# Kernel tuning notes

Measured on AMD Instinct MI355X. Metric: run time of the kernel, lower is better.

## Reference

```python
import jax, jax.numpy as jnp
import numpy as np

D_MODEL = 64
D_INNER = 128
D_STATE = 16
D_CONV = 4
DT_RANK = 4
P_PIX = 5
HH = 120
WW = 120


def _layernorm(x, g, b):
    m = x.mean(-1, keepdims=True)
    v = ((x - m) ** 2).mean(-1, keepdims=True)
    return (x - m) * jax.lax.rsqrt(v + 1e-5) * g + b


def _ssm_scan(delta, Bm, Cm, u, A):
    # delta,u: (b,L,d); Bm,Cm: (b,L,n); A: (d,n)
    def step(h, inp):
        dt, bt, ct, ut = inp  # (b,d),(b,n),(b,n),(b,d)
        h = h * jnp.exp(dt[:, :, None] * A) + (dt * ut)[:, :, None] * bt[:, None, :]
        return h, jnp.einsum('bdn,bn->bd', h, ct)
    h0 = jnp.zeros((u.shape[0], A.shape[0], A.shape[1]), u.dtype)
    xs = (jnp.swapaxes(delta, 0, 1), jnp.swapaxes(Bm, 0, 1),
          jnp.swapaxes(Cm, 0, 1), jnp.swapaxes(u, 0, 1))
    _, ys = jax.lax.scan(step, h0, xs)
    return jnp.swapaxes(ys, 0, 1)  # (b,L,d)


def _mamba(p, x):
    # faithful mamba_ssm Mamba with use_fast_path=False, out_proj=Identity
    in_w, conv_w, conv_b, xproj_w, dt_w, dt_b, A_log, Dv = p
    L = x.shape[1]
    xz = jnp.einsum('bld,ed->ble', x, in_w)  # (b,L,2*d_inner)
    xh, z = xz[..., :D_INNER], xz[..., D_INNER:]
    xp = jnp.pad(xh, ((0, 0), (D_CONV - 1, 0), (0, 0)))  # causal depthwise conv
    conv = conv_b + sum(xp[:, i:i + L, :] * conv_w[:, i] for i in range(D_CONV))
    xh = jax.nn.silu(conv)
    dbl = jnp.einsum('bld,ed->ble', xh, xproj_w)
    dt = dbl[..., :DT_RANK]
    Bm = dbl[..., DT_RANK:DT_RANK + D_STATE]
    Cm = dbl[..., DT_RANK + D_STATE:]
    delta = jax.nn.softplus(jnp.einsum('blr,dr->bld', dt, dt_w) + dt_b)
    A = -jnp.exp(A_log)
    y = _ssm_scan(delta, Bm, Cm, xh, A) + xh * Dv
    return y * jax.nn.silu(z)


def _bidir(p2, xn):
    inp = jnp.stack([xn, xn[:, ::-1]])  # forward + flipped sequence
    ys = jax.vmap(_mamba, in_axes=(0, 0))(p2, inp)
    return ys[0], ys[1]


def _pixel(x, p2, g, b, out_w):
    B, C, Hh, Ww = x.shape
    p = P_PIX
    NH, NW = Hh // p, Ww // p
    L = NH * NW
    xd = x.reshape(B, C, NH, p, NW, p).transpose(0, 3, 5, 1, 2, 4).reshape(B * p * p, C, L)
    xn = _layernorm(jnp.swapaxes(xd, 1, 2), g, b)
    yf, yb = _bidir(p2, xn)
    yo = jnp.einsum('bld,cd->blc', yf + yb[:, ::-1], out_w)
    xo = jnp.swapaxes(yo, 1, 2).reshape(B, p, p, C, NH, NW).transpose(0, 3, 4, 1, 5, 2).reshape(B, C, Hh, Ww)
    return xo + x


def _window(x, p2, g, b, out_w, out_bw):
    # window p==1: AvgPool(1)/Upsample(1) are identities
    B, C, Hh, Ww = x.shape
    L = Hh * Ww
    xn = _layernorm(jnp.swapaxes(x.reshape(B, C, L), 1, 2), g, b)
    yf, yb = _bidir(p2, xn)
    xM = jnp.einsum('bld,cd->bcl', yf, out_w)
    yM = jnp.einsum('bld,cd->bcl', yb, out_bw)
    xo = jnp.einsum('bld,cd->blc', yf + yb[:, ::-1], out_w)
    return jnp.swapaxes(xo, 1, 2).reshape(B, C, Hh, Ww) + x, xM, yM


def _edges(M, step=32):
    hub = np.arange(0, M, step)
    ii, jj = np.meshgrid(hub, hub, indexing='ij')
    mask = ii != jj
    # off-diagonal hub-hub edges + self loops for every node (GCNConv add_remaining_self_loops)
    src = np.concatenate([ii[mask], np.arange(M)])
    dst = np.concatenate([jj[mask], np.arange(M)])
    deg = np.bincount(dst, minlength=M).astype(np.float32)
    norm = (deg[src] ** -0.5) * (deg[dst] ** -0.5)
    return jnp.asarray(src), jnp.asarray(dst), jnp.asarray(norm, jnp.float32)


def _gcn(x, Wm, bv, src, dst, norm, M):
    h = jnp.einsum('bmf,gf->bmg', x, Wm)
    msg = h[:, src, :] * norm[None, :, None]          # (B,E,g)
    agg = jax.ops.segment_sum(jnp.swapaxes(msg, 0, 1), dst, num_segments=M)
    return jnp.swapaxes(agg, 0, 1) + bv


def setup_inputs() -> dict:
    key = jax.random.key(0)
    ks = iter(jax.random.split(key, 48))
    def rn(shape, scale=1.0):
        return jax.random.normal(next(ks), shape, jnp.float32) * scale
    d = {}
    d['x'] = rn((1, D_MODEL, HH, WW))
    for pre in ('pix', 'win'):
        d[pre + '_in_w'] = rn((4, 2, 2 * D_INNER, D_MODEL), D_MODEL ** -0.5)
        d[pre + '_conv_w'] = rn((4, 2, D_INNER, D_CONV), 0.3)
        d[pre + '_conv_b'] = rn((4, 2, D_INNER), 0.02)
        d[pre + '_xproj_w'] = rn((4, 2, DT_RANK + 2 * D_STATE, D_INNER), D_INNER ** -0.5)
        d[pre + '_dt_w'] = rn((4, 2, D_INNER, DT_RANK), DT_RANK ** -0.5)
        d[pre + '_dt_b'] = jax.random.uniform(next(ks), (4, 2, D_INNER), jnp.float32, -5.0, -3.0)
        d[pre + '_A_log'] = jnp.log(jax.random.uniform(next(ks), (4, 2, D_INNER, D_STATE), jnp.float32, 1.0, 16.0))
        d[pre + '_D'] = rn((4, 2, D_INNER), 0.5)
        d[pre + '_ln_g'] = jnp.ones((4, D_MODEL), jnp.float32)
        d[pre + '_ln_b'] = jnp.zeros((4, D_MODEL), jnp.float32)
    d['pix_out_w'] = rn((4, D_MODEL, D_INNER), D_INNER ** -0.5)
    d['win_out_w'] = rn((4, D_MODEL, D_INNER), D_INNER ** -0.5)
    d['win_out_bw'] = rn((4, D_MODEL, D_INNER), D_INNER ** -0.5)
    d['gcn_w1'] = rn((2 * D_MODEL, 4 * D_MODEL), (4 * D_MODEL) ** -0.5)
    d['gcn_b1'] = jnp.zeros((2 * D_MODEL,), jnp.float32)
    d['gcn_w2'] = rn((D_MODEL, 2 * D_MODEL), (2 * D_MODEL) ** -0.5)
    d['gcn_b2'] = jnp.zeros((D_MODEL,), jnp.float32)
    return d


def reference(x, pix_in_w, pix_conv_w, pix_conv_b, pix_xproj_w, pix_dt_w, pix_dt_b, pix_A_log, pix_D,
              win_in_w, win_conv_w, win_conv_b, win_xproj_w, win_dt_w, win_dt_b, win_A_log, win_D,
              pix_ln_g, pix_ln_b, win_ln_g, win_ln_b, pix_out_w, win_out_w, win_out_bw,
              gcn_w1, gcn_b1, gcn_w2, gcn_b2):
    pix_stack = (pix_in_w, pix_conv_w, pix_conv_b, pix_xproj_w, pix_dt_w, pix_dt_b, pix_A_log, pix_D)
    win_stack = (win_in_w, win_conv_w, win_conv_b, win_xproj_w, win_dt_w, win_dt_b, win_A_log, win_D)
    def pick(stack, i):
        return tuple(t[i] for t in stack)
    def branch(x0, base):
        lastx, xM, yM = x0, None, None
        for s in range(2):
            i = base + s
            a = _pixel(lastx, pick(pix_stack, i), pix_ln_g[i], pix_ln_b[i], pix_out_w[i])
            a, xM, yM = _window(a, pick(win_stack, i), win_ln_g[i], win_ln_b[i], win_out_w[i], win_out_bw[i])
            lastx = lastx + a
        return lastx, xM, yM
    old = x
    lastx, xM, yM = branch(x, 0)
    lastx_T, xMT, yMT = branch(jnp.swapaxes(x, 2, 3), 2)
    B, C, Hh, Ww = x.shape
    M = Hh * Ww
    nf = jnp.swapaxes(jnp.concatenate([xM, yM, xMT, yMT], axis=1), 1, 2)  # (B,M,4C)
    src, dst, norm = _edges(M)
    h = jax.nn.relu(_gcn(nf, gcn_w1, gcn_b1, src, dst, norm, M))
    g = _gcn(h, gcn_w2, gcn_b2, src, dst, norm, M)
    gcn_x = jnp.swapaxes(g, 1, 2).reshape(B, C, Hh, Ww)
    return gcn_x + old + lastx + jnp.swapaxes(lastx_T, 2, 3)
```

## Files before the change

kernel.cpp:

```cpp
#include <hip/hip_runtime.h>
#include <hip/hip_bf16.h>

#define MT 14400
#define WNC 300
#define WCL 48
#define PT 16

typedef unsigned short u16;

__device__ __forceinline__ float b2f(u16 u){
  union { unsigned int i; float f; } v; v.i = ((unsigned int)u) << 16; return v.f;
}
__device__ __forceinline__ u16 f2b(float f){
  union { unsigned int i; float f; } v; v.f = f;
  unsigned int x = v.i;
  return (u16)((x + 0x7fffu + ((x >> 16) & 1u)) >> 16);
}
__device__ __forceinline__ unsigned int pk2(float a, float b){
  return (unsigned int)f2b(a) | ((unsigned int)f2b(b) << 16);
}
__device__ __forceinline__ void st8(float* p, uint4 v){
  *(float4*)p = make_float4(b2f((u16)v.x), b2f((u16)(v.x >> 16)), b2f((u16)v.y), b2f((u16)(v.y >> 16)));
  *(float4*)(p + 4) = make_float4(b2f((u16)v.z), b2f((u16)(v.z >> 16)), b2f((u16)v.w), b2f((u16)(v.w >> 16)));
}
__device__ __forceinline__ float siluf(float x){ return x / (1.f + expf(-x)); }
__device__ __forceinline__ float softplusf(float x){ return (x > 20.f) ? x : log1pf(expf(x)); }

__global__ __launch_bounds__(256) void k_detect(const u16* __restrict__ a, int n, int* __restrict__ flag){
  __shared__ int found;
  if (threadIdx.x == 0) found = 0;
  __syncthreads();
  int f = 0;
  for (int i = threadIdx.x; i < n; i += 256){
    float v = b2f(a[i]);
    if (!(fabsf(v) <= 1e9f)) f = 1;
  }
  if (f) atomicOr(&found, 1);
  __syncthreads();
  if (threadIdx.x == 0) *flag = found;
}

struct PTab {
  const void* src[27];
  float* dst[27];
  int n[27];
  int neg[27];
};

__global__ __launch_bounds__(256) void k_cvt(PTab tb, const int* __restrict__ flag){
  int id = blockIdx.y;
  int n = tb.n[id];
  int fp32 = *flag;
  float* d = tb.dst[id];
  int ng = tb.neg[id];
  for (int i = blockIdx.x * 256 + threadIdx.x; i < n; i += gridDim.x * 256){
    float v = fp32 ? ((const float*)tb.src[id])[i] : b2f(((const u16*)tb.src[id])[i]);
    if (ng) v = -expf(v) * 1.4426950408889634f;
    d[i] = v;
  }
}

__global__ __launch_bounds__(256) void k_wtrans(const float* __restrict__ Wpix, const float* __restrict__ Wwin,
                                                float* __restrict__ WTpix, float* __restrict__ WTwin){
  int mat = blockIdx.y;
  const float* src = (mat < 8) ? (Wpix + (size_t)mat * 16384) : (Wwin + (size_t)(mat - 8) * 16384);
  float* dst = (mat < 8) ? (WTpix + (size_t)mat * 16384) : (WTwin + (size_t)(mat - 8) * 16384);
  int idx = blockIdx.x * 256 + threadIdx.x;
  int e = idx >> 6, k = idx & 63;
  dst[k * 256 + e] = src[idx];
}

__global__ __launch_bounds__(256) void k_gcn1w(const float* __restrict__ ow, const float* __restrict__ obw,
                                               const float* __restrict__ G1, float* __restrict__ W1c){
  int str = blockIdx.y;
  int g = str >> 1, d = str & 1;
  int i2 = g * 2 + 1;
  const float* W = (d ? obw : ow) + (size_t)(i2 * 64) * 128;
  int idx = blockIdx.x * 256 + threadIdx.x;
  int kk = idx >> 7, f = idx & 127;
  float acc = 0.f;
  #pragma unroll 8
  for (int c = 0; c < 64; c++)
    acc += W[(size_t)c * 128 + kk] * G1[(size_t)f * 256 + str * 64 + c];
  W1c[((size_t)str * 128 + kk) * 128 + f] = acc;
}

__global__ __launch_bounds__(256) void k_cvt_x(const void* __restrict__ x, float* __restrict__ imgA,
                                               const int* __restrict__ flag){
  int idx = blockIdx.x * 256 + threadIdx.x;
  int l = idx % MT, c = idx / MT;
  float v = (*flag) ? ((const float*)x)[idx] : b2f(((const u16*)x)[idx]);
  imgA[idx] = v;
  imgA[(size_t)64 * MT + (size_t)c * MT + (l % 120) * 120 + l / 120] = v;
}

__global__ __launch_bounds__(256) void k_prep_xn(const float* __restrict__ img, const float* __restrict__ lng,
                                                 const float* __restrict__ lnb, u16* __restrict__ xn,
                                                 int s, int pixelMode){
  int tid = threadIdx.x;
  int q = blockIdx.x * 4 + (tid >> 6);
  int c = tid & 63;
  int g = q / MT, t = q % MT;
  int hw;
  if (pixelMode){
    int b = t / 576, l = t % 576;
    int ph = b / 5, pw = b % 5, nh = l / 24, nw = l % 24;
    hw = (nh * 5 + ph) * 120 + (nw * 5 + pw);
  } else hw = t;
  float v = img[(size_t)g * 64 * MT + (size_t)c * MT + hw];
  float sm = v;
  #pragma unroll
  for (int m = 32; m >= 1; m >>= 1) sm += __shfl_xor(sm, m);
  float mean = sm * (1.f / 64.f);
  float dv = v - mean;
  float s2 = dv * dv;
  #pragma unroll
  for (int m = 32; m >= 1; m >>= 1) s2 += __shfl_xor(s2, m);
  float var = s2 * (1.f / 64.f);
  int i2 = g * 2 + s;
  float o = dv * rsqrtf(var + 1e-5f) * lng[i2 * 64 + c] + lnb[i2 * 64 + c];
  xn[(size_t)g * MT * 64 + (size_t)t * 64 + c] = f2b(o);
}

__global__ __launch_bounds__(256) void k_inproj(const u16* __restrict__ xn, const float* __restrict__ WT,
                                                u16* __restrict__ xh, u16* __restrict__ z,
                                                int s, int pixelMode){
  int gd = blockIdx.y, g = gd >> 1, dir = gd & 1;
  int i2 = (g * 2 + s) * 2 + dir;
  int ttile = blockIdx.x >> 1, ntile = blockIdx.x & 1;
  int t0 = ttile * 64;
  const float* WTm = WT + (size_t)i2 * 16384 + ntile * 128;

  __shared__ __align__(16) float sA[64 * 68];
  __shared__ __align__(16) float sB[64 * 128];
  int tid = threadIdx.x;

  {
    int k0 = (tid & 15) * 4;
    #pragma unroll
    for (int it = 0; it < 4; it++){
      int t = (tid >> 4) + it * 16;
      int tq = t0 + t, src = tq;
      if (dir){
        if (pixelMode){ int b = tq / 576, l = tq % 576; src = b * 576 + 575 - l; }
        else src = MT - 1 - tq;
      }
      uint2 v = *(const uint2*)&xn[(size_t)g * MT * 64 + (size_t)src * 64 + k0];
      sA[t * 68 + k0]     = b2f((u16)v.x);
      sA[t * 68 + k0 + 1] = b2f((u16)(v.x >> 16));
      sA[t * 68 + k0 + 2] = b2f((u16)v.y);
      sA[t * 68 + k0 + 3] = b2f((u16)(v.y >> 16));
    }
  }
  {
    #pragma unroll
    for (int it = 0; it < 8; it++){
      int idx = it * 256 + tid;
      int k = idx >> 5, e4 = (idx & 31) * 4;
      float4 v = *(const float4*)&WTm[(size_t)k * 256 + e4];
      *(float4*)&sB[k * 128 + e4] = v;
    }
  }
  __syncthreads();

  int tr = tid >> 4, tc = tid & 15;
  float acc[4][8];
  #pragma unroll
  for (int i = 0; i < 4; i++)
    #pragma unroll
    for (int j = 0; j < 8; j++) acc[i][j] = 0.f;

  for (int k0 = 0; k0 < 64; k0 += 4){
    float4 a4[4];
    #pragma unroll
    for (int i = 0; i < 4; i++) a4[i] = *(const float4*)&sA[(tr * 4 + i) * 68 + k0];
    #pragma unroll
    for (int kk = 0; kk < 4; kk++){
      float4 b0 = *(const float4*)&sB[(k0 + kk) * 128 + tc * 8];
      float4 b1 = *(const float4*)&sB[(k0 + kk) * 128 + tc * 8 + 4];
      float bv[8] = {b0.x, b0.y, b0.z, b0.w, b1.x, b1.y, b1.z, b1.w};
      #pragma unroll
      for (int i = 0; i < 4; i++){
        const float* ap = (const float*)&a4[i];
        float av = ap[kk];
        #pragma unroll
        for (int j = 0; j < 8; j++) acc[i][j] += av * bv[j];
      }
    }
  }

  u16* dst = ntile ? z : xh;
  #pragma unroll
  for (int i = 0; i < 4; i++){
    int t_out = t0 + tr * 4 + i;
    size_t base = (size_t)gd * MT * 128 + (size_t)t_out * 128 + tc * 8;
    uint4 o;
    o.x = pk2(acc[i][0], acc[i][1]); o.y = pk2(acc[i][2], acc[i][3]);
    o.z = pk2(acc[i][4], acc[i][5]); o.w = pk2(acc[i][6], acc[i][7]);
    *(uint4*)&dst[base] = o;
  }
}

__global__ __launch_bounds__(256) void k_conv(const u16* __restrict__ raw, const float* __restrict__ cw,
                                              const float* __restrict__ cb, u16* __restrict__ xhs,
                                              int s, int pixelMode){
  int gd = blockIdx.y, g = gd >> 1, dir = gd & 1;
  int i2 = (g * 2 + s) * 2 + dir;
  int idx = blockIdx.x * 256 + threadIdx.x;
  int t = idx >> 7, ch = idx & 127;
  int SL = pixelMode ? 576 : MT;
  int pos = t % SL;
  const u16* src = raw + (size_t)gd * MT * 128;
  const float* wrow = cw + (size_t)(i2 * 128 + ch) * 4;
  float acc = cb[i2 * 128 + ch];
  #pragma unroll
  for (int i = 0; i < 4; i++){
    int d = 3 - i;
    if (pos >= d) acc += b2f(src[(size_t)(t - d) * 128 + ch]) * wrow[i];
  }
  xhs[(size_t)gd * MT * 128 + idx] = f2b(siluf(acc));
}

__global__ __launch_bounds__(256) void k_xproj(const u16* __restrict__ xhs, const float* __restrict__ xpb,
                                               const float* __restrict__ dtw, const float* __restrict__ dtb,
                                               u16* __restrict__ delta, u16* __restrict__ Bm,
                                               u16* __restrict__ Cm, int s){
  int gd = blockIdx.y, g = gd >> 1, dir = gd & 1;
  int i2 = (g * 2 + s) * 2 + dir;
  const float* XP = xpb + (size_t)i2 * 36 * 128;
  const float* DW = dtw + (size_t)i2 * 128 * 4;
  const float* DB = dtb + (size_t)i2 * 128;
  int t0 = blockIdx.x * 64;
  size_t gb = (size_t)gd * MT * 128;
  size_t gb16 = (size_t)gd * MT * 16;

  __shared__ __align__(16) float sX[64 * 132];
  __shared__ __align__(16) float sW[48 * 132];
  float* sDbl = sX;
  int tid = threadIdx.x;

  #pragma unroll
  for (int it = 0; it < 8; it++){
    int idx = it * 256 + tid;
    int tok = idx >> 5, k4 = (idx & 31) * 4;
    uint2 v = *(const uint2*)&xhs[gb + (size_t)(t0 + tok) * 128 + k4];
    sX[tok * 132 + k4]     = b2f((u16)v.x);
    sX[tok * 132 + k4 + 1] = b2f((u16)(v.x >> 16));
    sX[tok * 132 + k4 + 2] = b2f((u16)v.y);
    sX[tok * 132 + k4 + 3] = b2f((u16)(v.y >> 16));
  }
  for (int idx = tid; idx < 48 * 32; idx += 256){
    int out = idx >> 5, k4 = (idx & 31) * 4;
    float4 v = (out < 36) ? *(const float4*)&XP[(size_t)out * 128 + k4]
                          : make_float4(0.f, 0.f, 0.f, 0.f);
    *(float4*)&sW[out * 132 + k4] = v;
  }
  __syncthreads();

  int tr = tid >> 4, tc = tid & 15;
  float acc[4][3];
  #pragma unroll
  for (int i = 0; i < 4; i++){ acc[i][0]=0.f; acc[i][1]=0.f; acc[i][2]=0.f; }

  for (int k0 = 0; k0 < 128; k0 += 4){
    float4 a4[4], bw[3];
    #pragma unroll
    for (int i = 0; i < 4; i++) a4[i] = *(const float4*)&sX[(tr * 4 + i) * 132 + k0];
    #pragma unroll
    for (int j = 0; j < 3; j++) bw[j] = *(const float4*)&sW[(tc * 3 + j) * 132 + k0];
    #pragma unroll
    for (int kk = 0; kk < 4; kk++){
      #pragma unroll
      for (int i = 0; i < 4; i++){
        float av = ((const float*)&a4[i])[kk];
        #pragma unroll
        for (int j = 0; j < 3; j++) acc[i][j] += av * ((const float*)&bw[j])[kk];
      }
    }
  }
  __syncthreads();

  #pragma unroll
  for (int i = 0; i < 4; i++){
    #pragma unroll
    for (int j = 0; j < 3; j++){
      int out = tc * 3 + j;
      if (out < 36) sDbl[(tr * 4 + i) * 52 + out] = acc[i][j];
    }
  }
  __syncthreads();

  {
    int d = tid & 127, half = tid >> 7;
    float4 dw = *(const float4*)&DW[(size_t)d * 4];
    float db = DB[d];
    #pragma unroll
    for (int it = 0; it < 32; it++){
      int t = it * 2 + half;
      const float* row = &sDbl[t * 52];
      float v = db + row[0] * dw.x + row[1] * dw.y + row[2] * dw.z + row[3] * dw.w;
      delta[gb + (size_t)(t0 + t) * 128 + d] = f2b(softplusf(v));
    }
  }
  #pragma unroll
  for (int it = 0; it < 8; it++){
    int flat = it * 256 + tid;
    int t = flat >> 5, n = flat & 31;
    float v = sDbl[t * 52 + 4 + n];
    if (n < 16) Bm[gb16 + (size_t)(t0 + t) * 16 + n] = f2b(v);
    else        Cm[gb16 + (size_t)(t0 + t) * 16 + (n - 16)] = f2b(v);
  }
}

__global__ __launch_bounds__(256) void k_scan_p1(const u16* __restrict__ delta, const u16* __restrict__ xhs,
                                                 const u16* __restrict__ Bm, const float* __restrict__ A2b,
                                                 float* __restrict__ Acar, float* __restrict__ Bcar, int s){
  int gd = blockIdx.y, g = gd >> 1, dir = gd & 1;
  int i2 = (g * 2 + s) * 2 + dir;
  int chunk = blockIdx.x;
  int tid = threadIdx.x, ch = tid >> 1, nb = (tid & 1) * 8;
  float A2[8], ap[8], bc[8];
  #pragma unroll
  for (int j = 0; j < 8; j++){
    A2[j] = A2b[((size_t)i2 * 128 + ch) * 16 + nb + j];
    ap[j] = 1.f; bc[j] = 0.f;
  }
  size_t so = (size_t)gd * MT * 128 + (size_t)chunk * WCL * 128;
  size_t bo = (size_t)gd * MT * 16  + (size_t)chunk * WCL * 16;
  __shared__ __align__(16) float sd[PT * 128];
  __shared__ __align__(16) float su[PT * 128];
  __shared__ __align__(16) float sb[PT * 16];
  uint4 rd, ru; float rbf;
  rd = *(const uint4*)&delta[so + 8 * (size_t)tid];
  ru = *(const uint4*)&xhs[so + 8 * (size_t)tid];
  rbf = b2f(Bm[bo + tid]);
  const int NT = WCL / PT;
  for (int tile = 0; tile < NT; tile++){
    __syncthreads();
    st8(&sd[8 * tid], rd);
    st8(&su[8 * tid], ru);
    sb[tid] = rbf;
    __syncthreads();
    if (tile + 1 < NT){
      rd = *(const uint4*)&delta[so + (size_t)(tile + 1) * PT * 128 + 8 * (size_t)tid];
      ru = *(const uint4*)&xhs[so + (size_t)(tile + 1) * PT * 128 + 8 * (size_t)tid];
      rbf = b2f(Bm[bo + (size_t)(tile + 1) * PT * 16 + tid]);
    }
    #pragma unroll
    for (int t = 0; t < PT; t++){
      float dt = sd[t * 128 + ch];
      float u  = su[t * 128 + ch];
      float du = dt * u;
      #pragma unroll
      for (int j = 0; j < 8; j++){
        float e = exp2f(dt * A2[j]);
        bc[j] = bc[j] * e + du * sb[t * 16 + nb + j];
        ap[j] *= e;
      }
    }
  }
  size_t o = ((size_t)gd * WNC + chunk) * 2048 + (size_t)ch * 16 + nb;
  float4* A4 = (float4*)(Acar + o);
  float4* B4 = (float4*)(Bcar + o);
  A4[0] = make_float4(ap[0], ap[1], ap[2], ap[3]);
  A4[1] = make_float4(ap[4], ap[5], ap[6], ap[7]);
  B4[0] = make_float4(bc[0], bc[1], bc[2], bc[3]);
  B4[1] = make_float4(bc[4], bc[5], bc[6], bc[7]);
}

__global__ __launch_bounds__(256) void k_scan_p2(const float* __restrict__ Acar, const float* __restrict__ Bcar,
                                                 float* __restrict__ Hin, int resetPeriod){
  int flat = blockIdx.x * 256 + threadIdx.x;
  int cs = flat & 2047, gd = flat >> 11;
  float h = 0.f;
  int cnt = 0;
  for (int c = 0; c < WNC; c++){
    if (cnt == resetPeriod) { h = 0.f; cnt = 0; }
    cnt++;
    size_t o = ((size_t)gd * WNC + c) * 2048 + cs;
    Hin[o] = h;
    h = Acar[o] * h + Bcar[o];
  }
}

__global__ __launch_bounds__(256) void k_scan_p3(const u16* __restrict__ delta, const u16* __restrict__ xhs,
                                                 const u16* __restrict__ Bm, const u16* __restrict__ Cm,
                                                 const u16* __restrict__ zz, const float* __restrict__ A2b,
                                                 const float* __restrict__ Db, const float* __restrict__ Hin,
                                                 u16* __restrict__ ys, int s){
  int gd = blockIdx.y, g = gd >> 1, dir = gd & 1;
  int i2 = (g * 2 + s) * 2 + dir;
  int chunk = blockIdx.x;
  int tid = threadIdx.x, ch = tid >> 1, nb = (tid & 1) * 8;
  float A2[8], h[8];
  size_t ho = ((size_t)gd * WNC + chunk) * 2048 + (size_t)ch * 16 + nb;
  {
    const float4* H4 = (const float4*)(Hin + ho);
    float4 h0 = H4[0], h1 = H4[1];
    h[0]=h0.x; h[1]=h0.y; h[2]=h0.z; h[3]=h0.w;
    h[4]=h1.x; h[5]=h1.y; h[6]=h1.z; h[7]=h1.w;
  }
  #pragma unroll
  for (int j = 0; j < 8; j++) A2[j] = A2b[((size_t)i2 * 128 + ch) * 16 + nb + j];
  float Dv = Db[(size_t)i2 * 128 + ch];
  size_t so = (size_t)gd * MT * 128 + (size_t)chunk * WCL * 128;
  size_t bo = (size_t)gd * MT * 16  + (size_t)chunk * WCL * 16;
  __shared__ __align__(16) float sd[PT * 128];
  __shared__ __align__(16) float su[PT * 128];
  __shared__ __align__(16) float sb[PT * 16];
  __shared__ __align__(16) float sc[PT * 16];
  __shared__ __align__(16) float sy[PT * 128];
  uint4 rd, ru; float rbf, rcf;
  rd = *(const uint4*)&delta[so + 8 * (size_t)tid];
  ru = *(const uint4*)&xhs[so + 8 * (size_t)tid];
  rbf = b2f(Bm[bo + tid]); rcf = b2f(Cm[bo + tid]);
  const int NT = WCL / PT;
  for (int tile = 0; tile < NT; tile++){
    __syncthreads();
    st8(&sd[8 * tid], rd);
    st8(&su[8 * tid], ru);
    sb[tid] = rbf; sc[tid] = rcf;
    __syncthreads();
    if (tile + 1 < NT){
      rd = *(const uint4*)&delta[so + (size_t)(tile + 1) * PT * 128 + 8 * (size_t)tid];
      ru = *(const uint4*)&xhs[so + (size_t)(tile + 1) * PT * 128 + 8 * (size_t)tid];
      rbf = b2f(Bm[bo + (size_t)(tile + 1) * PT * 16 + tid]);
      rcf = b2f(Cm[bo + (size_t)(tile + 1) * PT * 16 + tid]);
    }
    #pragma unroll
    for (int t = 0; t < PT; t++){
      float dt = sd[t * 128 + ch];
      float u  = su[t * 128 + ch];
      float du = dt * u;
      float acc = 0.f;
      #pragma unroll
      for (int j = 0; j < 8; j++){
        float e = exp2f(dt * A2[j]);
        h[j] = h[j] * e + du * sb[t * 16 + nb + j];
        acc += h[j] * sc[t * 16 + nb + j];
      }
      acc += __shfl_xor(acc, 1);
      if (!(tid & 1)) sy[t * 128 + ch] = acc + u * Dv;
    }
    __syncthreads();
    {
      uint4 zv = *(const uint4*)&zz[so + (size_t)tile * PT * 128 + 8 * (size_t)tid];
      const float* py = &sy[8 * tid];
      float y[8];
      y[0] = py[0] * siluf(b2f((u16)zv.x));       y[1] = py[1] * siluf(b2f((u16)(zv.x >> 16)));
      y[2] = py[2] * siluf(b2f((u16)zv.y));       y[3] = py[3] * siluf(b2f((u16)(zv.y >> 16)));
      y[4] = py[4] * siluf(b2f((u16)zv.z));       y[5] = py[5] * siluf(b2f((u16)(zv.z >> 16)));
      y[6] = py[6] * siluf(b2f((u16)zv.w));       y[7] = py[7] * siluf(b2f((u16)(zv.w >> 16)));
      uint4 o;
      o.x = pk2(y[0], y[1]); o.y = pk2(y[2], y[3]); o.z = pk2(y[4], y[5]); o.w = pk2(y[6], y[7]);
      *(uint4*)&ys[so + (size_t)tile * PT * 128 + 8 * (size_t)tid] = o;
    }
    __syncthreads();
  }
}

__global__ __launch_bounds__(256) void k_outproj_pixel(const u16* __restrict__ ys, const float* __restrict__ owb,
                                                       const float* __restrict__ imgA, float* __restrict__ imgB, int s){
  int g = blockIdx.y;
  int i2 = g * 2 + s;
  int tile = blockIdx.x;
  int t0 = tile * 64;
  int b = tile / 9, l0 = (tile % 9) * 64;
  const float* W = owb + (size_t)(i2 * 64) * 128;
  const u16* Yf = ys + (size_t)(g * 2 + 0) * MT * 128;
  const u16* Yb = ys + (size_t)(g * 2 + 1) * MT * 128;
  __shared__ __align__(16) float sA[64 * 36];
  __shared__ __align__(16) float sW[32 * 68];
  __shared__ __align__(16) float sO[64 * 68];
  int tid = threadIdx.x;
  int tr = tid >> 4, tc = tid & 15;
  float acc[4][4];
  #pragma unroll
  for (int i = 0; i < 4; i++){ acc[i][0]=0.f; acc[i][1]=0.f; acc[i][2]=0.f; acc[i][3]=0.f; }

  for (int kt = 0; kt < 4; kt++){
    int k0 = kt * 32;
    {
      int t = tid >> 2, f8 = (tid & 3) * 8;
      int rt = b * 576 + 575 - (l0 + t);
      uint4 vf = *(const uint4*)&Yf[(size_t)(t0 + t) * 128 + k0 + f8];
      uint4 vb = *(const uint4*)&Yb[(size_t)rt * 128 + k0 + f8];
      float* pa = &sA[t * 36 + f8];
      pa[0] = b2f((u16)vf.x) + b2f((u16)vb.x);
      pa[1] = b2f((u16)(vf.x >> 16)) + b2f((u16)(vb.x >> 16));
      pa[2] = b2f((u16)vf.y) + b2f((u16)vb.y);
      pa[3] = b2f((u16)(vf.y >> 16)) + b2f((u16)(vb.y >> 16));
      pa[4] = b2f((u16)vf.z) + b2f((u16)vb.z);
      pa[5] = b2f((u16)(vf.z >> 16)) + b2f((u16)(vb.z >> 16));
      pa[6] = b2f((u16)vf.w) + b2f((u16)vb.w);
      pa[7] = b2f((u16)(vf.w >> 16)) + b2f((u16)(vb.w >> 16));
    }
    {
      int c = tid >> 2, f8 = (tid & 3) * 8;
      const float* wr = &W[(size_t)c * 128 + k0 + f8];
      #pragma unroll
      for (int j = 0; j < 8; j++) sW[(f8 + j) * 68 + c] = wr[j];
    }
    __syncthreads();
    #pragma unroll
    for (int k4 = 0; k4 < 32; k4 += 4){
      float4 a[4];
      #pragma unroll
      for (int i = 0; i < 4; i++) a[i] = *(const float4*)&sA[(tr * 4 + i) * 36 + k4];
      #pragma unroll
      for (int kk = 0; kk < 4; kk++){
        float4 bv = *(const float4*)&sW[(k4 + kk) * 68 + tc * 4];
        #pragma unroll
        for (int i = 0; i < 4; i++){
          float av = ((const float*)&a[i])[kk];
          acc[i][0] += av * bv.x; acc[i][1] += av * bv.y;
          acc[i][2] += av * bv.z; acc[i][3] += av * bv.w;
        }
      }
    }
    __syncthreads();
  }
  #pragma unroll
  for (int j = 0; j < 4; j++)
    *(float4*)&sO[(tc * 4 + j) * 68 + tr * 4] = make_float4(acc[0][j], acc[1][j], acc[2][j], acc[3][j]);
  __syncthreads();
  {
    int c = tid >> 2, q = tid & 3;
    int ph = b / 5, pw = b % 5;
    size_t base = (size_t)g * 64 * MT + (size_t)c * MT;
    #pragma unroll
    for (int v = 0; v < 16; v++){
      int l = l0 + q * 16 + v;
      int nh = l / 24, nw = l % 24;
      size_t io = base + (nh * 5 + ph) * 120 + (nw * 5 + pw);
      imgB[io] = imgA[io] + sO[c * 68 + q * 16 + v];
    }
  }
}

__global__ __launch_bounds__(256) void k_outproj_win(const u16* __restrict__ ys, const float* __restrict__ owb,
                                                     float* __restrict__ imgA, float* __restrict__ imgB, int s){
  int g = blockIdx.y;
  int i2 = g * 2 + s;
  int t0 = blockIdx.x * 64;
  const float* W = owb + (size_t)(i2 * 64) * 128;
  const u16* Yf = ys + (size_t)(g * 2 + 0) * MT * 128;
  const u16* Yb = ys + (size_t)(g * 2 + 1) * MT * 128;
  __shared__ __align__(16) float sA[64 * 36];
  __shared__ __align__(16) float sW[32 * 68];
  __shared__ __align__(16) float sO[64 * 68];
  int tid = threadIdx.x;
  int tr = tid >> 4, tc = tid & 15;
  float acc[4][4];
  #pragma unroll
  for (int i = 0; i < 4; i++){ acc[i][0]=0.f; acc[i][1]=0.f; acc[i][2]=0.f; acc[i][3]=0.f; }

  for (int kt = 0; kt < 4; kt++){
    int k0 = kt * 32;
    {
      int t = tid >> 2, f8 = (tid & 3) * 8;
      int l = t0 + t;
      uint4 vf = *(const uint4*)&Yf[(size_t)l * 128 + k0 + f8];
      uint4 vb = *(const uint4*)&Yb[(size_t)(MT - 1 - l) * 128 + k0 + f8];
      float* pa = &sA[t * 36 + f8];
      pa[0] = b2f((u16)vf.x) + b2f((u16)vb.x);
      pa[1] = b2f((u16)(vf.x >> 16)) + b2f((u16)(vb.x >> 16));
      pa[2] = b2f((u16)vf.y) + b2f((u16)vb.y);
      pa[3] = b2f((u16)(vf.y >> 16)) + b2f((u16)(vb.y >> 16));
      pa[4] = b2f((u16)vf.z) + b2f((u16)vb.z);
      pa[5] = b2f((u16)(vf.z >> 16)) + b2f((u16)(vb.z >> 16));
      pa[6] = b2f((u16)vf.w) + b2f((u16)vb.w);
      pa[7] = b2f((u16)(vf.w >> 16)) + b2f((u16)(vb.w >> 16));
    }
    {
      int c = tid >> 2, f8 = (tid & 3) * 8;
      const float* wr = &W[(size_t)c * 128 + k0 + f8];
      #pragma unroll
      for (int j = 0; j < 8; j++) sW[(f8 + j) * 68 + c] = wr[j];
    }
    __syncthreads();
    #pragma unroll
    for (int k4 = 0; k4 < 32; k4 += 4){
      float4 a[4];
      #pragma unroll
      for (int i = 0; i < 4; i++) a[i] = *(const float4*)&sA[(tr * 4 + i) * 36 + k4];
      #pragma unroll
      for (int kk = 0; kk < 4; kk++){
        float4 bv = *(const float4*)&sW[(k4 + kk) * 68 + tc * 4];
        #pragma unroll
        for (int i = 0; i < 4; i++){
          float av = ((const float*)&a[i])[kk];
          acc[i][0] += av * bv.x; acc[i][1] += av * bv.y;
          acc[i][2] += av * bv.z; acc[i][3] += av * bv.w;
        }
      }
    }
    __syncthreads();
  }
  #pragma unroll
  for (int j = 0; j < 4; j++)
    *(float4*)&sO[(tc * 4 + j) * 68 + tr * 4] = make_float4(acc[0][j], acc[1][j], acc[2][j], acc[3][j]);
  __syncthreads();
  {
    int c = tid >> 2, q = tid & 3;
    size_t base = (size_t)g * 64 * MT + (size_t)c * MT + t0 + q * 16;
    float* pB = &imgB[base];
    float* pA = &imgA[base];
    const float* pS = &sO[c * 68 + q * 16];
    #pragma unroll
    for (int v = 0; v < 4; v++){
      float4 d = *(const float4*)&pS[v * 4];
      float4 bb = *(const float4*)&pB[v * 4];
      bb.x += d.x; bb.y += d.y; bb.z += d.z; bb.w += d.w;
      *(float4*)&pB[v * 4] = bb;
      float4 aa = *(const float4*)&pA[v * 4];
      aa.x += bb.x; aa.y += bb.y; aa.z += bb.z; aa.w += bb.w;
      *(float4*)&pA[v * 4] = aa;
    }
  }
}

__global__ __launch_bounds__(256) void k_gcn1(const u16* __restrict__ ys, const float* __restrict__ W1c,
                                              float* __restrict__ t1){
  int t0 = blockIdx.x * 64;
  __shared__ __align__(16) float sA[64 * 36];
  __shared__ __align__(16) float sB[32 * 132];
  int tid = threadIdx.x, tr = tid >> 4, tc = tid & 15;
  float acc[4][8];
  #pragma unroll
  for (int i = 0; i < 4; i++)
    #pragma unroll
    for (int j = 0; j < 8; j++) acc[i][j] = 0.f;

  for (int kt = 0; kt < 16; kt++){
    int str = kt >> 2, k0 = (kt & 3) * 32;
    const u16* Y = ys + (size_t)str * MT * 128;
    {
      int t = tid >> 2, f8 = (tid & 3) * 8;
      uint4 p = *(const uint4*)&Y[(size_t)(t0 + t) * 128 + k0 + f8];
      st8(&sA[t * 36 + f8], p);
    }
    {
      const float* Wc = W1c + ((size_t)str * 128 + k0) * 128;
      int kk = tid >> 3, f16 = (tid & 7) * 16;
      #pragma unroll
      for (int v = 0; v < 4; v++)
        *(float4*)&sB[kk * 132 + f16 + v * 4] = *(const float4*)&Wc[(size_t)kk * 128 + f16 + v * 4];
    }
    __syncthreads();
    #pragma unroll
    for (int k4 = 0; k4 < 32; k4 += 4){
      float4 a[4];
      #pragma unroll
      for (int i = 0; i < 4; i++) a[i] = *(const float4*)&sA[(tr * 4 + i) * 36 + k4];
      #pragma unroll
      for (int kk = 0; kk < 4; kk++){
        float4 b0 = *(const float4*)&sB[(k4 + kk) * 132 + tc * 8];
        float4 b1 = *(const float4*)&sB[(k4 + kk) * 132 + tc * 8 + 4];
        float bv[8] = {b0.x, b0.y, b0.z, b0.w, b1.x, b1.y, b1.z, b1.w};
        #pragma unroll
        for (int i = 0; i < 4; i++){
          float av = ((const float*)&a[i])[kk];
          #pragma unroll
          for (int j = 0; j < 8; j++) acc[i][j] += av * bv[j];
        }
      }
    }
    __syncthreads();
  }
  #pragma unroll
  for (int i = 0; i < 4; i++){
    size_t base = (size_t)(t0 + tr * 4 + i) * 128 + tc * 8;
    *(float4*)&t1[base]     = make_float4(acc[i][0], acc[i][1], acc[i][2], acc[i][3]);
    *(float4*)&t1[base + 4] = make_float4(acc[i][4], acc[i][5], acc[i][6], acc[i][7]);
  }
}

__global__ __launch_bounds__(128) void k_hub1(const float* __restrict__ t1, float* __restrict__ hubm){
  int f = threadIdx.x;
  float sum = 0.f;
  for (int hb = 0; hb < 450; hb++) sum += t1[(size_t)(hb * 32) * 128 + f];
  hubm[f] = sum * (1.f / 450.f);
}

__global__ __launch_bounds__(256) void k_gcn2(const float* __restrict__ t1, const float* __restrict__ hubm,
                                              const float* __restrict__ b1, const float* __restrict__ W2,
                                              float* __restrict__ t2){
  int t0 = blockIdx.x * 64;
  __shared__ __align__(16) float sA[64 * 36];
  __shared__ __align__(16) float sW[32 * 68];
  int tid = threadIdx.x, tr = tid >> 4, tc = tid & 15;
  float acc[4][4];
  #pragma unroll
  for (int i = 0; i < 4; i++){ acc[i][0]=0.f; acc[i][1]=0.f; acc[i][2]=0.f; acc[i][3]=0.f; }

  for (int kt = 0; kt < 4; kt++){
    int k0 = kt * 32;
    {
      int t = tid >> 2, f8 = (tid & 3) * 8;
      int l = t0 + t;
      const float* src = ((l & 31) == 0) ? &hubm[k0 + f8] : &t1[(size_t)l * 128 + k0 + f8];
      #pragma unroll
      for (int j = 0; j < 8; j++)
        sA[t * 36 + f8 + j] = fmaxf(src[j] + b1[k0 + f8 + j], 0.f);
    }
    {
      int c = tid >> 2, f8 = (tid & 3) * 8;
      const float* wr = &W2[(size_t)c * 128 + k0 + f8];
      #pragma unroll
      for (int j = 0; j < 8; j++) sW[(f8 + j) * 68 + c] = wr[j];
    }
    __syncthreads();
    #pragma unroll
    for (int k4 = 0; k4 < 32; k4 += 4){
      float4 a[4];
      #pragma unroll
      for (int i = 0; i < 4; i++) a[i] = *(const float4*)&sA[(tr * 4 + i) * 36 + k4];
      #pragma unroll
      for (int kk = 0; kk < 4; kk++){
        float4 bv = *(const float4*)&sW[(k4 + kk) * 68 + tc * 4];
        #pragma unroll
        for (int i = 0; i < 4; i++){
          float av = ((const float*)&a[i])[kk];
          acc[i][0] += av * bv.x; acc[i][1] += av * bv.y;
          acc[i][2] += av * bv.z; acc[i][3] += av * bv.w;
        }
      }
    }
    __syncthreads();
  }
  #pragma unroll
  for (int i = 0; i < 4; i++)
    *(float4*)&t2[(size_t)(t0 + tr * 4 + i) * 64 + tc * 4] = make_float4(acc[i][0], acc[i][1], acc[i][2], acc[i][3]);
}

__global__ __launch_bounds__(64) void k_hub2(const float* __restrict__ t2, float* __restrict__ hubm2){
  int c = threadIdx.x;
  float sum = 0.f;
  for (int hb = 0; hb < 450; hb++) sum += t2[(size_t)(hb * 32) * 64 + c];
  hubm2[c] = sum * (1.f / 450.f);
}

__global__ __launch_bounds__(256) void k_final(const void* __restrict__ x, const float* __restrict__ t2,
                                               const float* __restrict__ hubm2, const float* __restrict__ b2,
                                               const float* __restrict__ imgA, void* __restrict__ out,
                                               const int* __restrict__ flag){
  int idx = blockIdx.x * 256 + threadIdx.x;
  int l = idx % MT, c = idx / MT;
  int fp32 = *flag;
  float gval = (((l & 31) == 0) ? hubm2[c] : t2[(size_t)l * 64 + c]) + b2[c];
  float a0 = imgA[idx];
  float a1 = imgA[(size_t)64 * MT + (size_t)c * MT + (l % 120) * 120 + l / 120];
  float xv = fp32 ? ((const float*)x)[idx] : b2f(((const u16*)x)[idx]);
  float val = gval + xv + a0 + a1;
  if (fp32) ((float*)out)[idx] = val;
  else      ((u16*)out)[idx] = f2b(val);
}

extern "C" void kernel_launch(void* const* d_in, const int* in_sizes, int n_in,
                              void* d_out, int out_size, void* d_ws, size_t ws_size,
                              hipStream_t stream){
  int I_X=0,I_PIW=1,I_PCW=2,I_PCB=3,I_PXP=4,I_PDTW=5,I_PDTB=6,I_PAL=7,I_PD=8,I_PLG=9,I_PLB=10,
      I_WIW=11,I_WCW=12,I_WCB=13,I_WXP=14,I_WDTW=15,I_WDTB=16,I_WAL=17,I_WD=18,I_WLG=19,I_WLB=20,
      I_POW=21,I_WOW=22,I_WOBW=23,I_G1=24,I_GB1=25,I_G2=26,I_GB2=27;
  if (n_in >= 28 && in_sizes[9] == 131072){
    I_WIW=9;I_WCW=10;I_WCB=11;I_WXP=12;I_WDTW=13;I_WDTB=14;I_WAL=15;I_WD=16;
    I_PLG=17;I_PLB=18;I_WLG=19;I_WLB=20;
  }
  if (n_in < 28 || in_sizes[I_PIW] != 131072 || out_size != 921600) return;

  float* Wp = (float*)d_ws;
  size_t off = 0;
  auto alloc = [&](size_t n){ size_t r = off; off += (n + 63) & ~(size_t)63; return r; };
  size_t oFlag=alloc(64);
  size_t oPIW=alloc(131072), oPCW=alloc(4096), oPCB=alloc(1024), oPXP=alloc(36864),
         oPDTW=alloc(4096), oPDTB=alloc(1024), oPA=alloc(16384), oPD=alloc(1024),
         oPLG=alloc(256), oPLB=alloc(256);
  size_t oWIW=alloc(131072), oWCW=alloc(4096), oWCB=alloc(1024), oWXP=alloc(36864),
         oWDTW=alloc(4096), oWDTB=alloc(1024), oWA=alloc(16384), oWD=alloc(1024),
         oWLG=alloc(256), oWLB=alloc(256);
  size_t oPOW=alloc(32768), oWOW=alloc(32768), oWOBW=alloc(32768),
         oG1=alloc(32768), oGB1=alloc(128), oG2=alloc(8192), oGB2=alloc(64);
  size_t oPIWT=alloc(131072), oWIWT=alloc(131072), oW1C=alloc(65536);
  size_t oImgA=alloc(2UL*64*MT), oImgB=alloc(2UL*64*MT);
  size_t oXn=alloc((size_t)MT*64);
  size_t oRaw=alloc(2UL*MT*128);
  size_t oZ=alloc(2UL*MT*128), oXhs=alloc(2UL*MT*128), oDelta=alloc(2UL*MT*128);
  size_t oBm=alloc(2UL*MT*16), oCm=alloc(2UL*MT*16);
  size_t oAc=alloc(4UL*WNC*2048), oBc=alloc(4UL*WNC*2048), oHin=alloc(4UL*WNC*2048);
  size_t oT1=alloc((size_t)MT*128), oHub1=alloc(128), oT2=alloc((size_t)MT*64), oHub2=alloc(64);
  if (ws_size < off * sizeof(float)) return;

  int* flag = (int*)(Wp + oFlag);
  k_detect<<<dim3(1), dim3(256), 0, stream>>>((const u16*)d_in[I_PAL], 16384, flag);

  PTab tb;
  int ti = 0;
  auto add = [&](int inIdx, size_t o, int n, int neg){
    tb.src[ti] = d_in[inIdx]; tb.dst[ti] = Wp + o; tb.n[ti] = n; tb.neg[ti] = neg; ti++;
  };
  add(I_PIW,oPIW,131072,0); add(I_PCW,oPCW,4096,0); add(I_PCB,oPCB,1024,0); add(I_PXP,oPXP,36864,0);
  add(I_PDTW,oPDTW,4096,0); add(I_PDTB,oPDTB,1024,0); add(I_PAL,oPA,16384,1); add(I_PD,oPD,1024,0);
  add(I_PLG,oPLG,256,0); add(I_PLB,oPLB,256,0);
  add(I_WIW,oWIW,131072,0); add(I_WCW,oWCW,4096,0); add(I_WCB,oWCB,1024,0); add(I_WXP,oWXP,36864,0);
  add(I_WDTW,oWDTW,4096,0); add(I_WDTB,oWDTB,1024,0); add(I_WAL,oWA,16384,1); add(I_WD,oWD,1024,0);
  add(I_WLG,oWLG,256,0); add(I_WLB,oWLB,256,0);
  add(I_POW,oPOW,32768,0); add(I_WOW,oWOW,32768,0); add(I_WOBW,oWOBW,32768,0);
  add(I_G1,oG1,32768,0); add(I_GB1,oGB1,128,0); add(I_G2,oG2,8192,0); add(I_GB2,oGB2,64,0);

  k_cvt<<<dim3(128, 27), dim3(256), 0, stream>>>(tb, flag);
  k_wtrans<<<dim3(64, 16), dim3(256), 0, stream>>>(Wp+oPIW, Wp+oWIW, Wp+oPIWT, Wp+oWIWT);
  k_gcn1w<<<dim3(64, 4), dim3(256), 0, stream>>>(Wp+oWOW, Wp+oWOBW, Wp+oG1, Wp+oW1C);
  k_cvt_x<<<dim3(3600), dim3(256), 0, stream>>>(d_in[I_X], Wp + oImgA, flag);

  float *imgA = Wp+oImgA, *imgB = Wp+oImgB,
        *Ac = Wp+oAc, *Bc = Wp+oBc, *Hin = Wp+oHin;
  u16 *xn = (u16*)(Wp+oXn), *raw = (u16*)(Wp+oRaw), *ys = (u16*)(Wp+oRaw),
      *zz = (u16*)(Wp+oZ), *xhs = (u16*)(Wp+oXhs), *delta = (u16*)(Wp+oDelta),
      *Bm = (u16*)(Wp+oBm), *Cm = (u16*)(Wp+oCm);

  for (int s = 0; s < 2; s++){
    k_prep_xn<<<dim3(7200), dim3(256), 0, stream>>>(imgA, Wp+oPLG, Wp+oPLB, xn, s, 1);
    k_inproj <<<dim3(450, 4), dim3(256), 0, stream>>>(xn, Wp+oPIWT, raw, zz, s, 1);
    k_conv   <<<dim3(7200, 4), dim3(256), 0, stream>>>(raw, Wp+oPCW, Wp+oPCB, xhs, s, 1);
    k_xproj  <<<dim3(225, 4), dim3(256), 0, stream>>>(xhs, Wp+oPXP, Wp+oPDTW, Wp+oPDTB, delta, Bm, Cm, s);
    k_scan_p1<<<dim3(WNC, 4), dim3(256), 0, stream>>>(delta, xhs, Bm, Wp+oPA, Ac, Bc, s);
    k_scan_p2<<<dim3(32), dim3(256), 0, stream>>>(Ac, Bc, Hin, 12);
    k_scan_p3<<<dim3(WNC, 4), dim3(256), 0, stream>>>(delta, xhs, Bm, Cm, zz, Wp+oPA, Wp+oPD, Hin, ys, s);
    k_outproj_pixel<<<dim3(225, 2), dim3(256), 0, stream>>>(ys, Wp+oPOW, imgA, imgB, s);

    k_prep_xn<<<dim3(7200), dim3(256), 0, stream>>>(imgB, Wp+oWLG, Wp+oWLB, xn, s, 0);
    k_inproj <<<dim3(450, 4), dim3(256), 0, stream>>>(xn, Wp+oWIWT, raw, zz, s, 0);
    k_conv   <<<dim3(7200, 4), dim3(256), 0, stream>>>(raw, Wp+oWCW, Wp+oWCB, xhs, s, 0);
    k_xproj  <<<dim3(225, 4), dim3(256), 0, stream>>>(xhs, Wp+oWXP, Wp+oWDTW, Wp+oWDTB, delta, Bm, Cm, s);
    k_scan_p1<<<dim3(WNC, 4), dim3(256), 0, stream>>>(delta, xhs, Bm, Wp+oWA, Ac, Bc, s);
    k_scan_p2<<<dim3(32), dim3(256), 0, stream>>>(Ac, Bc, Hin, WNC);
    k_scan_p3<<<dim3(WNC, 4), dim3(256), 0, stream>>>(delta, xhs, Bm, Cm, zz, Wp+oWA, Wp+oWD, Hin, ys, s);
    k_outproj_win<<<dim3(225, 2), dim3(256), 0, stream>>>(ys, Wp+oWOW, imgA, imgB, s);
  }

  k_gcn1<<<dim3(225), dim3(256), 0, stream>>>(ys, Wp+oW1C, Wp+oT1);
  k_hub1<<<dim3(1), dim3(128), 0, stream>>>(Wp+oT1, Wp+oHub1);
  k_gcn2<<<dim3(225), dim3(256), 0, stream>>>(Wp+oT1, Wp+oHub1, Wp+oGB1, Wp+oG2, Wp+oT2);
  k_hub2<<<dim3(1), dim3(64), 0, stream>>>(Wp+oT2, Wp+oHub2);
  k_final<<<dim3(3600), dim3(256), 0, stream>>>(d_in[I_X], Wp+oT2, Wp+oHub2, Wp+oGB2, imgA, d_out, flag);
}
```

Before: 1.332 ms.

## Fuse layernorm into in-projection and causal conv into x-projection

Removes the separate layernorm and depthwise-conv kernels. Layernorm is now computed inside the in-projection tile load from the fp32 image, and the conv+SiLU is computed inside the x-projection tile load, which also writes xhs for the scan. This cuts four launches per stage and the round trips through the xn and xhs intermediates. In exchange, each in-projection block recomputes the layernorm for both N tiles and both directions, and its image reads are strided. The x-projection weight tile is also trimmed to 36 rows with clamped indices.

```diff
diff --git a/kernel.cpp b/kernel.cpp
--- a/kernel.cpp
+++ b/kernel.cpp
@@ -94,39 +94,13 @@
   imgA[(size_t)64 * MT + (size_t)c * MT + (l % 120) * 120 + l / 120] = v;
 }
 
-__global__ __launch_bounds__(256) void k_prep_xn(const float* __restrict__ img, const float* __restrict__ lng,
-                                                 const float* __restrict__ lnb, u16* __restrict__ xn,
-                                                 int s, int pixelMode){
-  int tid = threadIdx.x;
-  int q = blockIdx.x * 4 + (tid >> 6);
-  int c = tid & 63;
-  int g = q / MT, t = q % MT;
-  int hw;
-  if (pixelMode){
-    int b = t / 576, l = t % 576;
-    int ph = b / 5, pw = b % 5, nh = l / 24, nw = l % 24;
-    hw = (nh * 5 + ph) * 120 + (nw * 5 + pw);
-  } else hw = t;
-  float v = img[(size_t)g * 64 * MT + (size_t)c * MT + hw];
-  float sm = v;
-  #pragma unroll
-  for (int m = 32; m >= 1; m >>= 1) sm += __shfl_xor(sm, m);
-  float mean = sm * (1.f / 64.f);
-  float dv = v - mean;
-  float s2 = dv * dv;
-  #pragma unroll
-  for (int m = 32; m >= 1; m >>= 1) s2 += __shfl_xor(s2, m);
-  float var = s2 * (1.f / 64.f);
-  int i2 = g * 2 + s;
-  float o = dv * rsqrtf(var + 1e-5f) * lng[i2 * 64 + c] + lnb[i2 * 64 + c];
-  xn[(size_t)g * MT * 64 + (size_t)t * 64 + c] = f2b(o);
-}
-
-__global__ __launch_bounds__(256) void k_inproj(const u16* __restrict__ xn, const float* __restrict__ WT,
+__global__ __launch_bounds__(256) void k_inproj(const float* __restrict__ img, const float* __restrict__ lng,
+                                                const float* __restrict__ lnb, const float* __restrict__ WT,
                                                 u16* __restrict__ xh, u16* __restrict__ z,
                                                 int s, int pixelMode){
   int gd = blockIdx.y, g = gd >> 1, dir = gd & 1;
   int i2 = (g * 2 + s) * 2 + dir;
+  int iln = g * 2 + s;
   int ttile = blockIdx.x >> 1, ntile = blockIdx.x & 1;
   int t0 = ttile * 64;
   const float* WTm = WT + (size_t)i2 * 16384 + ntile * 128;
@@ -134,22 +108,44 @@
   __shared__ __align__(16) float sA[64 * 68];
   __shared__ __align__(16) float sB[64 * 128];
   int tid = threadIdx.x;
+  int row = tid >> 4, col = tid & 15;
 
   {
-    int k0 = (tid & 15) * 4;
+    const float* base = img + (size_t)g * 64 * MT;
+    float g0 = lng[iln * 64 + col * 4],     g1 = lng[iln * 64 + col * 4 + 1],
+          g2 = lng[iln * 64 + col * 4 + 2], g3 = lng[iln * 64 + col * 4 + 3];
+    float b0 = lnb[iln * 64 + col * 4],     b1 = lnb[iln * 64 + col * 4 + 1],
+          b2 = lnb[iln * 64 + col * 4 + 2], b3 = lnb[iln * 64 + col * 4 + 3];
     #pragma unroll
     for (int it = 0; it < 4; it++){
-      int t = (tid >> 4) + it * 16;
+      int t = row + it * 16;
       int tq = t0 + t, src = tq;
       if (dir){
         if (pixelMode){ int b = tq / 576, l = tq % 576; src = b * 576 + 575 - l; }
         else src = MT - 1 - tq;
       }
-      uint2 v = *(const uint2*)&xn[(size_t)g * MT * 64 + (size_t)src * 64 + k0];
-      sA[t * 68 + k0]     = b2f((u16)v.x);
-      sA[t * 68 + k0 + 1] = b2f((u16)(v.x >> 16));
-      sA[t * 68 + k0 + 2] = b2f((u16)v.y);
-      sA[t * 68 + k0 + 3] = b2f((u16)(v.y >> 16));
+      int hw;
+      if (pixelMode){
+        int b = src / 576, l = src % 576;
+        int ph = b / 5, pw = b % 5, nh = l / 24, nw = l % 24;
+        hw = (nh * 5 + ph) * 120 + (nw * 5 + pw);
+      } else hw = src;
+      float v0 = base[(size_t)(col * 4)     * MT + hw];
+      float v1 = base[(size_t)(col * 4 + 1) * MT + hw];
+      float v2 = base[(size_t)(col * 4 + 2) * MT + hw];
+      float v3 = base[(size_t)(col * 4 + 3) * MT + hw];
+      float sm = v0 + v1 + v2 + v3;
+      sm += __shfl_xor(sm, 1); sm += __shfl_xor(sm, 2);
+      sm += __shfl_xor(sm, 4); sm += __shfl_xor(sm, 8);
+      float mean = sm * (1.f / 64.f);
+      float d0 = v0 - mean, d1 = v1 - mean, d2 = v2 - mean, d3 = v3 - mean;
+      float s2 = d0 * d0 + d1 * d1 + d2 * d2 + d3 * d3;
+      s2 += __shfl_xor(s2, 1); s2 += __shfl_xor(s2, 2);
+      s2 += __shfl_xor(s2, 4); s2 += __shfl_xor(s2, 8);
+      float rs = rsqrtf(s2 * (1.f / 64.f) + 1e-5f);
+      float* pa = &sA[t * 68 + col * 4];
+      pa[0] = d0 * rs * g0 + b0; pa[1] = d1 * rs * g1 + b1;
+      pa[2] = d2 * rs * g2 + b2; pa[3] = d3 * rs * g3 + b3;
     }
   }
   {
@@ -201,41 +197,26 @@
   }
 }
 
-__global__ __launch_bounds__(256) void k_conv(const u16* __restrict__ raw, const float* __restrict__ cw,
-                                              const float* __restrict__ cb, u16* __restrict__ xhs,
-                                              int s, int pixelMode){
-  int gd = blockIdx.y, g = gd >> 1, dir = gd & 1;
-  int i2 = (g * 2 + s) * 2 + dir;
-  int idx = blockIdx.x * 256 + threadIdx.x;
-  int t = idx >> 7, ch = idx & 127;
-  int SL = pixelMode ? 576 : MT;
-  int pos = t % SL;
-  const u16* src = raw + (size_t)gd * MT * 128;
-  const float* wrow = cw + (size_t)(i2 * 128 + ch) * 4;
-  float acc = cb[i2 * 128 + ch];
-  #pragma unroll
-  for (int i = 0; i < 4; i++){
-    int d = 3 - i;
-    if (pos >= d) acc += b2f(src[(size_t)(t - d) * 128 + ch]) * wrow[i];
-  }
-  xhs[(size_t)gd * MT * 128 + idx] = f2b(siluf(acc));
-}
-
-__global__ __launch_bounds__(256) void k_xproj(const u16* __restrict__ xhs, const float* __restrict__ xpb,
+__global__ __launch_bounds__(256) void k_xproj(const u16* __restrict__ raw, const float* __restrict__ cw,
+                                               const float* __restrict__ cb, const float* __restrict__ xpb,
                                                const float* __restrict__ dtw, const float* __restrict__ dtb,
                                                u16* __restrict__ delta, u16* __restrict__ Bm,
-                                               u16* __restrict__ Cm, int s){
+                                               u16* __restrict__ Cm, u16* __restrict__ xhs,
+                                               int s, int pixelMode){
   int gd = blockIdx.y, g = gd >> 1, dir = gd & 1;
   int i2 = (g * 2 + s) * 2 + dir;
   const float* XP = xpb + (size_t)i2 * 36 * 128;
   const float* DW = dtw + (size_t)i2 * 128 * 4;
   const float* DB = dtb + (size_t)i2 * 128;
   int t0 = blockIdx.x * 64;
+  int SL = pixelMode ? 576 : MT;
+  int posBase = t0 % SL;
   size_t gb = (size_t)gd * MT * 128;
   size_t gb16 = (size_t)gd * MT * 16;
+  const u16* rawg = raw + gb;
 
   __shared__ __align__(16) float sX[64 * 132];
-  __shared__ __align__(16) float sW[48 * 132];
+  __shared__ __align__(16) float sW[36 * 132];
   float* sDbl = sX;
   int tid = threadIdx.x;
 
@@ -243,17 +224,33 @@
   for (int it = 0; it < 8; it++){
     int idx = it * 256 + tid;
     int tok = idx >> 5, k4 = (idx & 31) * 4;
-    uint2 v = *(const uint2*)&xhs[gb + (size_t)(t0 + tok) * 128 + k4];
-    sX[tok * 132 + k4]     = b2f((u16)v.x);
-    sX[tok * 132 + k4 + 1] = b2f((u16)(v.x >> 16));
-    sX[tok * 132 + k4 + 2] = b2f((u16)v.y);
-    sX[tok * 132 + k4 + 3] = b2f((u16)(v.y >> 16));
-  }
-  for (int idx = tid; idx < 48 * 32; idx += 256){
+    int t = t0 + tok, pos = posBase + tok;
+    const float4* wr0 = (const float4*)&cw[(size_t)(i2 * 128 + k4) * 4];
+    float4 w0 = wr0[0], w1 = wr0[1], w2 = wr0[2], w3 = wr0[3];
+    float4 cbv = *(const float4*)&cb[i2 * 128 + k4];
+    float a0 = cbv.x, a1 = cbv.y, a2 = cbv.z, a3 = cbv.w;
+    #pragma unroll
+    for (int i = 0; i < 4; i++){
+      int d = 3 - i;
+      if (pos >= d){
+        uint2 rv = *(const uint2*)&rawg[(size_t)(t - d) * 128 + k4];
+        float r0 = b2f((u16)rv.x), r1 = b2f((u16)(rv.x >> 16));
+        float r2 = b2f((u16)rv.y), r3 = b2f((u16)(rv.y >> 16));
+        a0 += r0 * ((const float*)&w0)[i];
+        a1 += r1 * ((const float*)&w1)[i];
+        a2 += r2 * ((const float*)&w2)[i];
+        a3 += r3 * ((const float*)&w3)[i];
+      }
+    }
+    a0 = siluf(a0); a1 = siluf(a1); a2 = siluf(a2); a3 = siluf(a3);
+    sX[tok * 132 + k4] = a0; sX[tok * 132 + k4 + 1] = a1;
+    sX[tok * 132 + k4 + 2] = a2; sX[tok * 132 + k4 + 3] = a3;
+    uint2 o; o.x = pk2(a0, a1); o.y = pk2(a2, a3);
+    *(uint2*)&xhs[gb + (size_t)t * 128 + k4] = o;
+  }
+  for (int idx = tid; idx < 36 * 32; idx += 256){
     int out = idx >> 5, k4 = (idx & 31) * 4;
-    float4 v = (out < 36) ? *(const float4*)&XP[(size_t)out * 128 + k4]
-                          : make_float4(0.f, 0.f, 0.f, 0.f);
-    *(float4*)&sW[out * 132 + k4] = v;
+    *(float4*)&sW[out * 132 + k4] = *(const float4*)&XP[(size_t)out * 128 + k4];
   }
   __syncthreads();
 
@@ -261,13 +258,17 @@
   float acc[4][3];
   #pragma unroll
   for (int i = 0; i < 4; i++){ acc[i][0]=0.f; acc[i][1]=0.f; acc[i][2]=0.f; }
+  int o0 = tc * 3;     if (o0 > 35) o0 = 35;
+  int o1 = tc * 3 + 1; if (o1 > 35) o1 = 35;
+  int o2 = tc * 3 + 2; if (o2 > 35) o2 = 35;
 
   for (int k0 = 0; k0 < 128; k0 += 4){
     float4 a4[4], bw[3];
     #pragma unroll
     for (int i = 0; i < 4; i++) a4[i] = *(const float4*)&sX[(tr * 4 + i) * 132 + k0];
-    #pragma unroll
-    for (int j = 0; j < 3; j++) bw[j] = *(const float4*)&sW[(tc * 3 + j) * 132 + k0];
+    bw[0] = *(const float4*)&sW[o0 * 132 + k0];
+    bw[1] = *(const float4*)&sW[o1 * 132 + k0];
+    bw[2] = *(const float4*)&sW[o2 * 132 + k0];
     #pragma unroll
     for (int kk = 0; kk < 4; kk++){
       #pragma unroll
@@ -783,7 +784,6 @@
          oG1=alloc(32768), oGB1=alloc(128), oG2=alloc(8192), oGB2=alloc(64);
   size_t oPIWT=alloc(131072), oWIWT=alloc(131072), oW1C=alloc(65536);
   size_t oImgA=alloc(2UL*64*MT), oImgB=alloc(2UL*64*MT);
-  size_t oXn=alloc((size_t)MT*64);
   size_t oRaw=alloc(2UL*MT*128);
   size_t oZ=alloc(2UL*MT*128), oXhs=alloc(2UL*MT*128), oDelta=alloc(2UL*MT*128);
   size_t oBm=alloc(2UL*MT*16), oCm=alloc(2UL*MT*16);
@@ -815,24 +815,22 @@
 
   float *imgA = Wp+oImgA, *imgB = Wp+oImgB,
         *Ac = Wp+oAc, *Bc = Wp+oBc, *Hin = Wp+oHin;
-  u16 *xn = (u16*)(Wp+oXn), *raw = (u16*)(Wp+oRaw), *ys = (u16*)(Wp+oRaw),
+  u16 *raw = (u16*)(Wp+oRaw), *ys = (u16*)(Wp+oRaw),
       *zz = (u16*)(Wp+oZ), *xhs = (u16*)(Wp+oXhs), *delta = (u16*)(Wp+oDelta),
       *Bm = (u16*)(Wp+oBm), *Cm = (u16*)(Wp+oCm);
 
   for (int s = 0; s < 2; s++){
-    k_prep_xn<<<dim3(7200), dim3(256), 0, stream>>>(imgA, Wp+oPLG, Wp+oPLB, xn, s, 1);
-    k_inproj <<<dim3(450, 4), dim3(256), 0, stream>>>(xn, Wp+oPIWT, raw, zz, s, 1);
-    k_conv   <<<dim3(7200, 4), dim3(256), 0, stream>>>(raw, Wp+oPCW, Wp+oPCB, xhs, s, 1);
-    k_xproj  <<<dim3(225, 4), dim3(256), 0, stream>>>(xhs, Wp+oPXP, Wp+oPDTW, Wp+oPDTB, delta, Bm, Cm, s);
+    k_inproj<<<dim3(450, 4), dim3(256), 0, stream>>>(imgA, Wp+oPLG, Wp+oPLB, Wp+oPIWT, raw, zz, s, 1);
+    k_xproj <<<dim3(225, 4), dim3(256), 0, stream>>>(raw, Wp+oPCW, Wp+oPCB, Wp+oPXP, Wp+oPDTW, Wp+oPDTB,
+                                                     delta, Bm, Cm, xhs, s, 1);
     k_scan_p1<<<dim3(WNC, 4), dim3(256), 0, stream>>>(delta, xhs, Bm, Wp+oPA, Ac, Bc, s);
     k_scan_p2<<<dim3(32), dim3(256), 0, stream>>>(Ac, Bc, Hin, 12);
     k_scan_p3<<<dim3(WNC, 4), dim3(256), 0, stream>>>(delta, xhs, Bm, Cm, zz, Wp+oPA, Wp+oPD, Hin, ys, s);
     k_outproj_pixel<<<dim3(225, 2), dim3(256), 0, stream>>>(ys, Wp+oPOW, imgA, imgB, s);
 
-    k_prep_xn<<<dim3(7200), dim3(256), 0, stream>>>(imgB, Wp+oWLG, Wp+oWLB, xn, s, 0);
-    k_inproj <<<dim3(450, 4), dim3(256), 0, stream>>>(xn, Wp+oWIWT, raw, zz, s, 0);
-    k_conv   <<<dim3(7200, 4), dim3(256), 0, stream>>>(raw, Wp+oWCW, Wp+oWCB, xhs, s, 0);
-    k_xproj  <<<dim3(225, 4), dim3(256), 0, stream>>>(xhs, Wp+oWXP, Wp+oWDTW, Wp+oWDTB, delta, Bm, Cm, s);
+    k_inproj<<<dim3(450, 4), dim3(256), 0, stream>>>(imgB, Wp+oWLG, Wp+oWLB, Wp+oWIWT, raw, zz, s, 0);
+    k_xproj <<<dim3(225, 4), dim3(256), 0, stream>>>(raw, Wp+oWCW, Wp+oWCB, Wp+oWXP, Wp+oWDTW, Wp+oWDTB,
+                                                     delta, Bm, Cm, xhs, s, 0);
     k_scan_p1<<<dim3(WNC, 4), dim3(256), 0, stream>>>(delta, xhs, Bm, Wp+oWA, Ac, Bc, s);
     k_scan_p2<<<dim3(32), dim3(256), 0, stream>>>(Ac, Bc, Hin, WNC);
     k_scan_p3<<<dim3(WNC, 4), dim3(256), 0, stream>>>(delta, xhs, Bm, Cm, zz, Wp+oWA, Wp+oWD, Hin, ys, s);
```

Measured after the change: 1.240 ms. 1.07x faster.
